# Optimization experiments

Measured on AMD Instinct MI355X. Metric: run time of the kernel, lower is better.

## Reference

```python
import jax, jax.numpy as jnp
import numpy as np

D_MODEL = 768
D_STATE = 16
D_CONV = 4
EXPAND = 2
D_INNER = D_MODEL * EXPAND  # 1536
B = 2
T = 8192
ALPHA = 0.9  # hard-coded EMA coefficient in _parallel_scan


def setup_inputs() -> dict:
    key = jax.random.key(0)
    ks = jax.random.split(key, 12)
    s = 0.02
    return {
        "x": jax.random.normal(ks[0], (B, T, D_MODEL), jnp.float32),
        "in_w": jax.random.normal(ks[1], (D_MODEL, 2 * D_INNER), jnp.float32) * s,
        "in_b": jnp.zeros((2 * D_INNER,), jnp.float32),
        "conv_w": jax.random.normal(ks[2], (D_INNER, 1, D_CONV), jnp.float32) * s,  # OIH, depthwise
        "conv_b": jnp.zeros((D_INNER,), jnp.float32),
        "xp_w": jax.random.normal(ks[3], (D_INNER, 2 * D_STATE), jnp.float32) * s,
        "xp_b": jnp.zeros((2 * D_STATE,), jnp.float32),
        "dt_w": jax.random.normal(ks[4], (D_STATE, D_INNER), jnp.float32) * s,
        "dt_b": jnp.zeros((D_INNER,), jnp.float32),
        "D_param": jnp.ones((D_INNER,), jnp.float32),
        "out_w": jax.random.normal(ks[5], (D_INNER, D_MODEL), jnp.float32) * s,
        "out_b": jnp.zeros((D_MODEL,), jnp.float32),
    }


def _forward(x, in_w, in_b, conv_w, conv_b, xp_w, xp_b, dt_w, dt_b, D_param, out_w, out_b):
    # in_proj: [B,T,D] -> [B,T,2*d_inner]
    xz = x @ in_w + in_b
    x_inner, z = jnp.split(xz, 2, axis=-1)

    # Causal depthwise conv1d (torch pads both sides by d_conv-1 then slices [:T],
    # which is equivalent to left-pad d_conv-1, right-pad 0)
    xc = jnp.transpose(x_inner, (0, 2, 1))  # [B, d_inner, T]
    xc = jax.lax.conv_general_dilated(
        xc, conv_w, window_strides=(1,), padding=[(D_CONV - 1, 0)],
        dimension_numbers=("NCH", "OIH", "NCH"), feature_group_count=D_INNER,
    ) + conv_b[None, :, None]
    x_conv = jax.nn.silu(jnp.transpose(xc, (0, 2, 1)))  # [B, T, d_inner]

    # NOTE: original computes x_proj/dt_proj/A_bar here, but _parallel_scan ignores
    # A_bar/B_ssm/C_ssm entirely, so they are dead code w.r.t. the output (omitted).

    # Serial EMA scan: h_t = alpha*h_{t-1} + (1-alpha)*x_conv_t
    def step(h, xt):
        h = ALPHA * h + (1.0 - ALPHA) * xt
        return h, h

    h0 = jnp.zeros((x.shape[0], D_INNER), x_conv.dtype)
    _, hs = jax.lax.scan(step, h0, jnp.transpose(x_conv, (1, 0, 2)))  # [T,B,d_inner]
    scan_out = jnp.transpose(hs, (1, 0, 2))

    y = x_conv * D_param + scan_out
    y = y * jax.nn.silu(z)
    return y @ out_w + out_b  # dropout is identity at inference


def reference(x, in_w, in_b, conv_w, conv_b, xp_w, xp_b, dt_w, dt_b, D_param, out_w, out_b):
    return _forward(x, in_w, in_b, conv_w, conv_b, xp_w, xp_b, dt_w, dt_b, D_param, out_w, out_b)
```

## Files before the change

### kernel.cpp

```cpp
#include <hip/hip_runtime.h>

#define D_MODEL 768
#define D_INNER 1536
#define NXZ     3072
#define BATCH   2
#define SEQ     8192
#define MTOT    (BATCH*SEQ)
#define WARM    64

typedef _Float16 v8h __attribute__((ext_vector_type(8)));
typedef _Float16 v4h __attribute__((ext_vector_type(4)));
typedef float    v4f __attribute__((ext_vector_type(4)));
typedef _Float16 f16;

__global__ void k_cvt(const float* __restrict__ in, f16* __restrict__ out, int n4) {
  int i = blockIdx.x * blockDim.x + threadIdx.x;
  if (i < n4) {
    float4 v = reinterpret_cast<const float4*>(in)[i];
    v4h o;
    o[0] = (f16)v.x; o[1] = (f16)v.y; o[2] = (f16)v.z; o[3] = (f16)v.w;
    reinterpret_cast<v4h*>(out)[i] = o;
  }
}

__global__ void k_transpose_cvt(const float* __restrict__ in, f16* __restrict__ out,
                                int R, int C) {
  __shared__ float tile[32][33];
  int c0 = blockIdx.x * 32, r0 = blockIdx.y * 32;
  int tx = threadIdx.x, ty = threadIdx.y;
#pragma unroll
  for (int i = 0; i < 32; i += 8)
    tile[ty + i][tx] = in[(long)(r0 + ty + i) * C + (c0 + tx)];
  __syncthreads();
#pragma unroll
  for (int i = 0; i < 32; i += 8)
    out[(long)(c0 + ty + i) * R + (r0 + tx)] = (f16)tile[tx][ty + i];
}

__device__ __forceinline__ void gload_lds16(const void* g, void* l) {
  __builtin_amdgcn_global_load_lds((const __attribute__((address_space(1))) void*)g,
                                   (__attribute__((address_space(3))) void*)l, 16, 0, 0);
}

template <bool F16OUT>
__launch_bounds__(256, 2)
__global__ void k_gemm_bt(const f16* __restrict__ A, const f16* __restrict__ Bt,
                          const float* __restrict__ bias, void* __restrict__ Cv,
                          int M, int N, int K) {
  __shared__ f16 As[128][64];
  __shared__ f16 Bs[128][64];
  const int tid  = threadIdx.x;
  const int lane = tid & 63;
  const int wave = tid >> 6;
  const int wm   = (wave >> 1) * 64;
  const int wn   = (wave & 1) * 64;
  const int m16  = lane & 15;
  const int quad = lane >> 4;
  const long m0 = (long)blockIdx.y * 128;
  const long n0 = (long)blockIdx.x * 128;

  v4f acc[4][4];
#pragma unroll
  for (int i = 0; i < 4; i++)
#pragma unroll
    for (int j = 0; j < 4; j++)
#pragma unroll
      for (int r = 0; r < 4; r++) acc[i][j][r] = 0.f;

  const int  srow = wave * 8 + (lane >> 3);
  const int  gcol = ((lane & 7) ^ (lane >> 3)) << 3;
  const f16* Ag = A  + (m0 + srow) * (long)K + gcol;
  const f16* Bg = Bt + (n0 + srow) * (long)K + gcol;

  const int c0q = ((quad ^ (m16 & 7)) << 3);
  const int c1q = c0q ^ 32;

  for (int k0 = 0; k0 < K; k0 += 64) {
#pragma unroll
    for (int g = 0; g < 4; ++g) {
      gload_lds16(Ag + (long)(g * 32) * K, &As[wave * 8 + g * 32][0]);
      gload_lds16(Bg + (long)(g * 32) * K, &Bs[wave * 8 + g * 32][0]);
    }
    Ag += 64; Bg += 64;
    __syncthreads();
    v8h af[4], bfr[4];
#pragma unroll
    for (int i = 0; i < 4; i++) af[i]  = *(const v8h*)&As[wm + i * 16 + m16][c0q];
#pragma unroll
    for (int j = 0; j < 4; j++) bfr[j] = *(const v8h*)&Bs[wn + j * 16 + m16][c0q];
#pragma unroll
    for (int i = 0; i < 4; i++)
#pragma unroll
      for (int j = 0; j < 4; j++)
        acc[i][j] = __builtin_amdgcn_mfma_f32_16x16x32_f16(af[i], bfr[j], acc[i][j], 0, 0, 0);
#pragma unroll
    for (int i = 0; i < 4; i++) af[i]  = *(const v8h*)&As[wm + i * 16 + m16][c1q];
#pragma unroll
    for (int j = 0; j < 4; j++) bfr[j] = *(const v8h*)&Bs[wn + j * 16 + m16][c1q];
#pragma unroll
    for (int i = 0; i < 4; i++)
#pragma unroll
      for (int j = 0; j < 4; j++)
        acc[i][j] = __builtin_amdgcn_mfma_f32_16x16x32_f16(af[i], bfr[j], acc[i][j], 0, 0, 0);
    __syncthreads();
  }

#pragma unroll
  for (int i = 0; i < 4; i++) {
#pragma unroll
    for (int j = 0; j < 4; j++) {
      const long n = n0 + wn + j * 16 + m16;
      const float bv = bias[n];
#pragma unroll
      for (int r = 0; r < 4; r++) {
        const long m = m0 + wm + i * 16 + quad * 4 + r;
        float v = acc[i][j][r] + bv;
        if (F16OUT) ((f16*)Cv)[m * N + n] = (f16)v;
        else        ((float*)Cv)[m * N + n] = v;
      }
    }
  }
}

template <bool F16OUT>
__launch_bounds__(256, 2)
__global__ void k_gemm_big(const f16* __restrict__ A, const f16* __restrict__ Bt,
                           const float* __restrict__ bias, void* __restrict__ Cv,
                           int M, int N, int K) {
  __shared__ f16 As[256][64];
  __shared__ f16 Bs[128][64];
  const int tid  = threadIdx.x;
  const int lane = tid & 63;
  const int wave = tid >> 6;
  const int wm   = (wave >> 1) * 128;
  const int wn   = (wave & 1) * 64;
  const int m16  = lane & 15;
  const int quad = lane >> 4;
  const long m0 = (long)blockIdx.y * 256;
  const long n0 = (long)blockIdx.x * 128;

  v4f acc[8][4];
#pragma unroll
  for (int i = 0; i < 8; i++)
#pragma unroll
    for (int j = 0; j < 4; j++)
#pragma unroll
      for (int r = 0; r < 4; r++) acc[i][j][r] = 0.f;

  const int  srow = wave * 8 + (lane >> 3);
  const int  gcol = ((lane & 7) ^ (lane >> 3)) << 3;
  const f16* Ag = A  + (m0 + srow) * (long)K + gcol;
  const f16* Bg = Bt + (n0 + srow) * (long)K + gcol;
  f16* AsW = &As[wave * 8][0];
  f16* BsW = &Bs[wave * 8][0];

  const int c0q = ((quad ^ (m16 & 7)) << 3);
  const int c1q = c0q ^ 32;

  for (int k0 = 0; k0 < K; k0 += 64) {
#pragma unroll
    for (int g = 0; g < 8; ++g)
      gload_lds16(Ag + (long)(g * 32) * K, AsW + g * 32 * 64);
#pragma unroll
    for (int g = 0; g < 4; ++g)
      gload_lds16(Bg + (long)(g * 32) * K, BsW + g * 32 * 64);
    Ag += 64; Bg += 64;
    __syncthreads();
    v8h bfr[4], af;
#pragma unroll
    for (int j = 0; j < 4; j++) bfr[j] = *(const v8h*)&Bs[wn + j * 16 + m16][c0q];
#pragma unroll
    for (int i = 0; i < 8; i++) {
      af = *(const v8h*)&As[wm + i * 16 + m16][c0q];
#pragma unroll
      for (int j = 0; j < 4; j++)
        acc[i][j] = __builtin_amdgcn_mfma_f32_16x16x32_f16(af, bfr[j], acc[i][j], 0, 0, 0);
    }
#pragma unroll
    for (int j = 0; j < 4; j++) bfr[j] = *(const v8h*)&Bs[wn + j * 16 + m16][c1q];
#pragma unroll
    for (int i = 0; i < 8; i++) {
      af = *(const v8h*)&As[wm + i * 16 + m16][c1q];
#pragma unroll
      for (int j = 0; j < 4; j++)
        acc[i][j] = __builtin_amdgcn_mfma_f32_16x16x32_f16(af, bfr[j], acc[i][j], 0, 0, 0);
    }
    __syncthreads();
  }

#pragma unroll
  for (int i = 0; i < 8; i++) {
#pragma unroll
    for (int j = 0; j < 4; j++) {
      const long n = n0 + wn + j * 16 + m16;
      const float bv = bias[n];
#pragma unroll
      for (int r = 0; r < 4; r++) {
        const long m = m0 + wm + i * 16 + quad * 4 + r;
        float v = acc[i][j][r] + bv;
        if (F16OUT) ((f16*)Cv)[m * N + n] = (f16)v;
        else        ((float*)Cv)[m * N + n] = v;
      }
    }
  }
}

__global__ void k_conv_scan(const f16* __restrict__ xz, const float* __restrict__ conv_w,
                            const float* __restrict__ conv_b, const float* __restrict__ Dp_,
                            f16* __restrict__ y) {
  __shared__ f16 xs[64][256];
  __shared__ f16 zs[64][256];
  const int tid = threadIdx.x;
  const int c0  = blockIdx.y * 256;
  const int c   = c0 + tid;
  const int b   = blockIdx.z;
  const int t0  = blockIdx.x * 128;
  const float w0 = conv_w[c * 4 + 0], w1 = conv_w[c * 4 + 1];
  const float w2 = conv_w[c * 4 + 2], w3 = conv_w[c * 4 + 3];
  const float cb = conv_b[c], Dp = Dp_[c];
  const long mb = (long)b * SEQ;

  float xm3 = 0.f, xm2 = 0.f, xm1 = 0.f, h = 0.f;
  const int ts = t0 - WARM;
  if (t0 > 0) {
    xm3 = (float)xz[(mb + ts - 3) * (long)NXZ + c];
    xm2 = (float)xz[(mb + ts - 2) * (long)NXZ + c];
    xm1 = (float)xz[(mb + ts - 1) * (long)NXZ + c];
  }

  for (int p = 0; p < 3; ++p) {
    const int tp = ts + p * 64;
    __syncthreads();
    if (tp >= 0) {
#pragma unroll
      for (int j = 0; j < 8; ++j) {
        const int idx = j * 256 + tid, row = idx >> 5, col = (idx & 31) << 3;
        *(v8h*)&xs[row][col] = *(const v8h*)&xz[(mb + tp + row) * (long)NXZ + c0 + col];
      }
      if (p > 0) {
#pragma unroll
        for (int j = 0; j < 8; ++j) {
          const int idx = j * 256 + tid, row = idx >> 5, col = (idx & 31) << 3;
          *(v8h*)&zs[row][col] = *(const v8h*)&xz[(mb + tp + row) * (long)NXZ + D_INNER + c0 + col];
        }
      }
    }
    __syncthreads();
    if (tp < 0) continue;
    if (p == 0) {
#pragma unroll 8
      for (int tl = 0; tl < 64; ++tl) {
        float xt = (float)xs[tl][tid];
        float u = w0 * xm3 + w1 * xm2 + w2 * xm1 + w3 * xt + cb;
        h = 0.9f * h + 0.1f * (u / (1.f + __expf(-u)));
        xm3 = xm2; xm2 = xm1; xm1 = xt;
      }
    } else {
      f16* yo = y + (mb + tp) * (long)D_INNER + c;
#pragma unroll 8
      for (int tl = 0; tl < 64; ++tl) {
        float xt = (float)xs[tl][tid];
        float u = w0 * xm3 + w1 * xm2 + w2 * xm1 + w3 * xt + cb;
        float v = u / (1.f + __expf(-u));
        h = 0.9f * h + 0.1f * v;
        float zv = (float)zs[tl][tid];
        float g = zv / (1.f + __expf(-zv));
        yo[(long)tl * D_INNER] = (f16)((v * Dp + h) * g);
        xm3 = xm2; xm2 = xm1; xm1 = xt;
      }
    }
  }
}

extern "C" void kernel_launch(void* const* d_in, const int* in_sizes, int n_in,
                              void* d_out, int out_size, void* d_ws, size_t ws_size,
                              hipStream_t stream) {
  const float* x       = (const float*)d_in[0];
  const float* in_w    = (const float*)d_in[1];
  const float* in_b    = (const float*)d_in[2];
  const float* conv_w  = (const float*)d_in[3];
  const float* conv_b  = (const float*)d_in[4];
  const float* D_param = (const float*)d_in[9];
  const float* out_w   = (const float*)d_in[10];
  const float* out_b   = (const float*)d_in[11];
  float* out = (float*)d_out;

  char* p = (char*)d_ws;
  f16* xb    = (f16*)p; p += (size_t)MTOT * D_MODEL * 2;
  f16* wInT  = (f16*)p; p += (size_t)NXZ * D_MODEL * 2;
  f16* wOutT = (f16*)p; p += (size_t)D_MODEL * D_INNER * 2;
  f16* xzb   = (f16*)p; p += (size_t)MTOT * NXZ * 2;
  f16* yb    = (f16*)p; p += (size_t)MTOT * D_INNER * 2;

  k_cvt<<<(MTOT * D_MODEL / 4 + 255) / 256, 256, 0, stream>>>(x, xb, MTOT * D_MODEL / 4);
  k_transpose_cvt<<<dim3(NXZ / 32, D_MODEL / 32), dim3(32, 8), 0, stream>>>(in_w, wInT, D_MODEL, NXZ);
  k_transpose_cvt<<<dim3(D_MODEL / 32, D_INNER / 32), dim3(32, 8), 0, stream>>>(out_w, wOutT, D_INNER, D_MODEL);

  k_gemm_bt<true><<<dim3(NXZ / 128, MTOT / 128), 256, 0, stream>>>(xb, wInT, in_b, xzb, MTOT, NXZ, D_MODEL);

  k_conv_scan<<<dim3(SEQ / 128, D_INNER / 256, BATCH), 256, 0, stream>>>(xzb, conv_w, conv_b, D_param, yb);

  k_gemm_big<false><<<dim3(D_MODEL / 128, MTOT / 256), 256, 0, stream>>>(yb, wOutT, out_b, out, MTOT, D_MODEL, D_INNER);
}
```

Baseline: 339.1 us.

## Fuse prep kernels, drop LDS staging in conv-scan, use fast reciprocal silu

Merges the fp32-to-fp16 conversion and the two weight transposes into one launch, cutting kernel launch overhead. The conv-scan kernel no longer stages tiles through shared memory with barriers; each thread reads its own column straight from global memory, relying on the 256 threads of a block covering contiguous channels so that row accesses still coalesce. SiLU now uses a hardware v_rcp_f32 instead of a division, which is cheaper but slightly less accurate.

```diff
diff --git a/kernel.cpp b/kernel.cpp
--- a/kernel.cpp
+++ b/kernel.cpp
@@ -13,21 +13,25 @@
 typedef float    v4f __attribute__((ext_vector_type(4)));
 typedef _Float16 f16;
 
-__global__ void k_cvt(const float* __restrict__ in, f16* __restrict__ out, int n4) {
-  int i = blockIdx.x * blockDim.x + threadIdx.x;
-  if (i < n4) {
-    float4 v = reinterpret_cast<const float4*>(in)[i];
-    v4h o;
-    o[0] = (f16)v.x; o[1] = (f16)v.y; o[2] = (f16)v.z; o[3] = (f16)v.w;
-    reinterpret_cast<v4h*>(out)[i] = o;
-  }
-}
-
-__global__ void k_transpose_cvt(const float* __restrict__ in, f16* __restrict__ out,
-                                int R, int C) {
+__device__ __forceinline__ float frcp(float x) {
+  float r;
+  asm volatile("v_rcp_f32 %0, %1" : "=v"(r) : "v"(x));
+  return r;
+}
+__device__ __forceinline__ float fsilu(float u) {
+  return u * frcp(1.f + __expf(-u));
+}
+
+#define NCVT (MTOT * D_MODEL / 4 / 256)
+#define NT1  ((NXZ / 32) * (D_MODEL / 32))
+#define NT2  ((D_MODEL / 32) * (D_INNER / 32))
+
+__device__ __forceinline__ void transpose_tile(const float* __restrict__ in,
+                                               f16* __restrict__ out,
+                                               int R, int C, int bx, int by, int tid) {
   __shared__ float tile[32][33];
-  int c0 = blockIdx.x * 32, r0 = blockIdx.y * 32;
-  int tx = threadIdx.x, ty = threadIdx.y;
+  const int c0 = bx * 32, r0 = by * 32;
+  const int tx = tid & 31, ty = tid >> 5;
 #pragma unroll
   for (int i = 0; i < 32; i += 8)
     tile[ty + i][tx] = in[(long)(r0 + ty + i) * C + (c0 + tx)];
@@ -35,6 +39,26 @@
 #pragma unroll
   for (int i = 0; i < 32; i += 8)
     out[(long)(c0 + ty + i) * R + (r0 + tx)] = (f16)tile[tx][ty + i];
+}
+
+__global__ void k_prep(const float* __restrict__ x, f16* __restrict__ xb,
+                       const float* __restrict__ in_w, f16* __restrict__ wInT,
+                       const float* __restrict__ out_w, f16* __restrict__ wOutT) {
+  const int bid = blockIdx.x;
+  const int tid = threadIdx.x;
+  if (bid < NCVT) {
+    const int i = bid * 256 + tid;
+    float4 v = reinterpret_cast<const float4*>(x)[i];
+    v4h o;
+    o[0] = (f16)v.x; o[1] = (f16)v.y; o[2] = (f16)v.z; o[3] = (f16)v.w;
+    reinterpret_cast<v4h*>(xb)[i] = o;
+  } else if (bid < NCVT + NT1) {
+    const int b2 = bid - NCVT;
+    transpose_tile(in_w, wInT, D_MODEL, NXZ, b2 % (NXZ / 32), b2 / (NXZ / 32), tid);
+  } else {
+    const int b2 = bid - NCVT - NT1;
+    transpose_tile(out_w, wOutT, D_INNER, D_MODEL, b2 % (D_MODEL / 32), b2 / (D_MODEL / 32), tid);
+  }
 }
 
 __device__ __forceinline__ void gload_lds16(const void* g, void* l) {
@@ -208,11 +232,8 @@
 __global__ void k_conv_scan(const f16* __restrict__ xz, const float* __restrict__ conv_w,
                             const float* __restrict__ conv_b, const float* __restrict__ Dp_,
                             f16* __restrict__ y) {
-  __shared__ f16 xs[64][256];
-  __shared__ f16 zs[64][256];
   const int tid = threadIdx.x;
-  const int c0  = blockIdx.y * 256;
-  const int c   = c0 + tid;
+  const int c   = blockIdx.y * 256 + tid;
   const int b   = blockIdx.z;
   const int t0  = blockIdx.x * 128;
   const float w0 = conv_w[c * 4 + 0], w1 = conv_w[c * 4 + 1];
@@ -220,55 +241,36 @@
   const float cb = conv_b[c], Dp = Dp_[c];
   const long mb = (long)b * SEQ;
 
+  const f16* xcol = xz + mb * (long)NXZ + c;
+  const f16* zcol = xcol + D_INNER;
+  f16*       ycol = y  + mb * (long)D_INNER + c;
+
   float xm3 = 0.f, xm2 = 0.f, xm1 = 0.f, h = 0.f;
-  const int ts = t0 - WARM;
+  int ts = t0 - WARM;
   if (t0 > 0) {
-    xm3 = (float)xz[(mb + ts - 3) * (long)NXZ + c];
-    xm2 = (float)xz[(mb + ts - 2) * (long)NXZ + c];
-    xm1 = (float)xz[(mb + ts - 1) * (long)NXZ + c];
-  }
-
-  for (int p = 0; p < 3; ++p) {
-    const int tp = ts + p * 64;
-    __syncthreads();
-    if (tp >= 0) {
-#pragma unroll
-      for (int j = 0; j < 8; ++j) {
-        const int idx = j * 256 + tid, row = idx >> 5, col = (idx & 31) << 3;
-        *(v8h*)&xs[row][col] = *(const v8h*)&xz[(mb + tp + row) * (long)NXZ + c0 + col];
-      }
-      if (p > 0) {
-#pragma unroll
-        for (int j = 0; j < 8; ++j) {
-          const int idx = j * 256 + tid, row = idx >> 5, col = (idx & 31) << 3;
-          *(v8h*)&zs[row][col] = *(const v8h*)&xz[(mb + tp + row) * (long)NXZ + D_INNER + c0 + col];
-        }
-      }
-    }
-    __syncthreads();
-    if (tp < 0) continue;
-    if (p == 0) {
+    xm3 = (float)xcol[(long)(ts - 3) * NXZ];
+    xm2 = (float)xcol[(long)(ts - 2) * NXZ];
+    xm1 = (float)xcol[(long)(ts - 1) * NXZ];
+  } else {
+    ts = 0;
+  }
+
 #pragma unroll 8
-      for (int tl = 0; tl < 64; ++tl) {
-        float xt = (float)xs[tl][tid];
-        float u = w0 * xm3 + w1 * xm2 + w2 * xm1 + w3 * xt + cb;
-        h = 0.9f * h + 0.1f * (u / (1.f + __expf(-u)));
-        xm3 = xm2; xm2 = xm1; xm1 = xt;
-      }
-    } else {
-      f16* yo = y + (mb + tp) * (long)D_INNER + c;
+  for (int t = ts; t < t0; ++t) {
+    float xt = (float)xcol[(long)t * NXZ];
+    float u  = w0 * xm3 + w1 * xm2 + w2 * xm1 + w3 * xt + cb;
+    h = 0.9f * h + 0.1f * fsilu(u);
+    xm3 = xm2; xm2 = xm1; xm1 = xt;
+  }
 #pragma unroll 8
-      for (int tl = 0; tl < 64; ++tl) {
-        float xt = (float)xs[tl][tid];
-        float u = w0 * xm3 + w1 * xm2 + w2 * xm1 + w3 * xt + cb;
-        float v = u / (1.f + __expf(-u));
-        h = 0.9f * h + 0.1f * v;
-        float zv = (float)zs[tl][tid];
-        float g = zv / (1.f + __expf(-zv));
-        yo[(long)tl * D_INNER] = (f16)((v * Dp + h) * g);
-        xm3 = xm2; xm2 = xm1; xm1 = xt;
-      }
-    }
+  for (int t = t0; t < t0 + 128; ++t) {
+    float xt = (float)xcol[(long)t * NXZ];
+    float zv = (float)zcol[(long)t * NXZ];
+    float u  = w0 * xm3 + w1 * xm2 + w2 * xm1 + w3 * xt + cb;
+    float v  = fsilu(u);
+    h = 0.9f * h + 0.1f * v;
+    ycol[(long)t * D_INNER] = (f16)((v * Dp + h) * fsilu(zv));
+    xm3 = xm2; xm2 = xm1; xm1 = xt;
   }
 }
 
@@ -292,9 +294,7 @@
   f16* xzb   = (f16*)p; p += (size_t)MTOT * NXZ * 2;
   f16* yb    = (f16*)p; p += (size_t)MTOT * D_INNER * 2;
 
-  k_cvt<<<(MTOT * D_MODEL / 4 + 255) / 256, 256, 0, stream>>>(x, xb, MTOT * D_MODEL / 4);
-  k_transpose_cvt<<<dim3(NXZ / 32, D_MODEL / 32), dim3(32, 8), 0, stream>>>(in_w, wInT, D_MODEL, NXZ);
-  k_transpose_cvt<<<dim3(D_MODEL / 32, D_INNER / 32), dim3(32, 8), 0, stream>>>(out_w, wOutT, D_INNER, D_MODEL);
+  k_prep<<<NCVT + NT1 + NT2, 256, 0, stream>>>(x, xb, in_w, wInT, out_w, wOutT);
 
   k_gemm_bt<true><<<dim3(NXZ / 128, MTOT / 128), 256, 0, stream>>>(xb, wInT, in_b, xzb, MTOT, NXZ, D_MODEL);
 
```

New measurement: 340.7 us. No clear change (+0.5%).
